# Kernel tuning notes

Measured on AMD Instinct MI355X. Metric: run time of the kernel, lower is better.

Reference implementation:

```python
import jax, jax.numpy as jnp
import numpy as np

# Model config (matches init_kwargs)
DIM = 2048
INTER = 1408          # moe_inter_dim
E = 16                # n_routed_experts
TOPK = 4              # n_activated_experts
G = 4                 # n_expert_groups
TOPK_G = 2            # n_limited_groups
N_SHARED = 2
SHARED_INTER = N_SHARED * INTER  # 2816
ROUTE_SCALE = 1.0


def setup_inputs() -> dict:
    key = jax.random.key(0)
    ks = jax.random.split(key, 8)
    s = 0.02
    x = jax.random.normal(ks[0], (1, 2048, DIM), dtype=jnp.float32)
    Wg = jax.random.normal(ks[1], (E, DIM), dtype=jnp.float32) * s      # gate weight
    W1 = jax.random.normal(ks[2], (E, INTER, DIM), dtype=jnp.float32) * s  # expert gate proj
    W3 = jax.random.normal(ks[3], (E, INTER, DIM), dtype=jnp.float32) * s  # expert up proj
    W2 = jax.random.normal(ks[4], (E, DIM, INTER), dtype=jnp.float32) * s  # expert down proj
    Ws1 = jax.random.normal(ks[5], (SHARED_INTER, DIM), dtype=jnp.float32) * s
    Ws3 = jax.random.normal(ks[6], (SHARED_INTER, DIM), dtype=jnp.float32) * s
    Ws2 = jax.random.normal(ks[7], (DIM, SHARED_INTER), dtype=jnp.float32) * s
    return {"x": x, "Wg": Wg, "W1": W1, "W3": W3, "W2": W2,
            "Ws1": Ws1, "Ws3": Ws3, "Ws2": Ws2}


def _moe_forward(x, Wg, W1, W3, W2, Ws1, Ws3, Ws2):
    B, S, D = x.shape
    xt = x.reshape(-1, D)              # [T, D]
    T = xt.shape[0]

    # ---- Gate: group-limited top-k routing (bias is None since dim != 7168) ----
    scores = jax.nn.softmax(xt @ Wg.T, axis=-1)          # [T, E]
    sg = scores.reshape(T, G, E // G)                    # [T, G, E/G]
    group_scores = sg.max(axis=-1)                       # amax per group
    gidx = jax.lax.top_k(group_scores, TOPK_G)[1]        # [T, TOPK_G]
    gmask = jax.nn.one_hot(gidx, G, dtype=jnp.float32).sum(axis=1) > 0  # [T, G] kept groups
    masked = jnp.where(gmask[:, :, None], sg, -jnp.inf).reshape(T, E)
    topi = jax.lax.top_k(masked, TOPK)[1]                # [T, TOPK] expert indices
    weights = jnp.take_along_axis(scores, topi, axis=1) * ROUTE_SCALE  # original_scores gather

    # ---- Routed experts: dense per-expert SwiGLU FFN, zero-weight combine ----
    # combine[t, e] = sum over k of weights[t, k] * (topi[t, k] == e)
    combine = jnp.zeros((T, E), xt.dtype).at[jnp.arange(T)[:, None], topi].add(weights)
    h = jax.nn.silu(jnp.einsum('td,eid->eti', xt, W1)) * jnp.einsum('td,eid->eti', xt, W3)
    expert_out = jnp.einsum('eti,edi->etd', h, W2)       # [E, T, D]
    y = jnp.einsum('etd,te->td', expert_out, combine)    # [T, D]

    # ---- Shared expert (applied to all tokens) ----
    z = (jax.nn.silu(xt @ Ws1.T) * (xt @ Ws3.T)) @ Ws2.T

    return (y + z).reshape(B, S, D)


def reference(x, Wg, W1, W3, W2, Ws1, Ws3, Ws2):
    return _moe_forward(x, Wg, W1, W3, W2, Ws1, Ws3, Ws2)
```

## Files before the change

kernel.cpp:

```cpp
#include <hip/hip_runtime.h>
#include <stdint.h>

#define D_MODEL  2048
#define N_INTER  1408
#define N_EXP    16
#define SH_INTER 2816
#define T_TOK    2048

typedef __attribute__((ext_vector_type(8))) short bf16x8;
typedef __attribute__((ext_vector_type(4))) float f32x4;

__device__ __forceinline__ unsigned short f2bf(float f){
  unsigned int b = __builtin_bit_cast(unsigned int, f);
  b = (b + 0x7FFFu + ((b >> 16) & 1u)) >> 16;
  return (unsigned short)b;
}

__global__ void cvt_bf16_kernel(const float* __restrict__ x,
                                unsigned short* __restrict__ o, int n4){
  const int i = blockIdx.x * blockDim.x + threadIdx.x;
  if (i >= n4) return;
  const float4 v = ((const float4*)x)[i];
  ushort4 u; u.x = f2bf(v.x); u.y = f2bf(v.y); u.z = f2bf(v.z); u.w = f2bf(v.w);
  ((ushort4*)o)[i] = u;
}

__global__ void gate_kernel(const float* __restrict__ x, const float* __restrict__ Wg,
                            int* __restrict__ cnt, int* __restrict__ list,
                            float* __restrict__ wlist){
  const int t = blockIdx.x;
  const int l = threadIdx.x;
  const int e = l & 15, q = l >> 4;
  const float* xr = x + (size_t)t * D_MODEL + q * 512;
  const float* wr = Wg + (size_t)e * D_MODEL + q * 512;
  float p = 0.f;
  #pragma unroll 4
  for (int i = 0; i < 512; i += 4){
    float4 xv = *(const float4*)(xr + i);
    float4 wv = *(const float4*)(wr + i);
    p += xv.x*wv.x + xv.y*wv.y + xv.z*wv.z + xv.w*wv.w;
  }
  p += __shfl_xor(p, 16);
  p += __shfl_xor(p, 32);
  float mx = p;
  for (int d = 1; d < 16; d <<= 1) mx = fmaxf(mx, __shfl_xor(mx, d));
  float ex = __expf(p - mx);
  float sum = ex;
  for (int d = 1; d < 16; d <<= 1) sum += __shfl_xor(sum, d);
  const float sc = ex / sum;
  float gm = fmaxf(sc, __shfl_xor(sc, 1));
  gm = fmaxf(gm, __shfl_xor(gm, 2));
  const float g0 = __shfl(gm, 0), g1 = __shfl(gm, 4),
              g2 = __shfl(gm, 8), g3 = __shfl(gm, 12);
  const int grp = e >> 2;
  const float gs[4] = {g0, g1, g2, g3};
  int grank = 0;
  #pragma unroll
  for (int j = 0; j < 4; ++j)
    if (gs[j] > gm || (gs[j] == gm && j < grp)) grank++;
  const float msc = (grank < 2) ? sc : -INFINITY;
  int erank = 0;
  #pragma unroll
  for (int j = 0; j < 16; ++j){
    const float oj = __shfl(msc, j);
    if (oj > msc || (oj == msc && j < e)) erank++;
  }
  if (q == 0 && erank < 4 && msc > -INFINITY){
    const int pos = atomicAdd(&cnt[e], 1);
    list[e * T_TOK + pos]  = (t << 2) | erank;
    wlist[e * T_TOK + pos] = sc;
  }
}

template<int MODE>
__global__ __launch_bounds__(256, 2)
void gemm_kernel(const unsigned short* __restrict__ A,
                 const float* __restrict__ B1,
                 const float* __restrict__ B3,
                 void* __restrict__ OutP,
                 const int* __restrict__ list,
                 const int* __restrict__ cnt,
                 const float* __restrict__ wlist,
                 int N, int K, int MT, int NT)
{
  constexpr bool GU     = (MODE == 0 || MODE == 1);
  constexpr bool GATHER = (MODE == 1 || MODE == 3);

  __shared__ unsigned short As [128 * 40];
  __shared__ unsigned short Bs1[128 * 40];
  __shared__ unsigned short Bs3[GU ? 128 * 40 : 8];

  const int nb  = gridDim.x;
  const int per = nb >> 3;
  const int gsw = (blockIdx.x & 7) * per + (blockIdx.x >> 3);
  const int mt   = gsw % MT;
  const int rest = gsw / MT;
  int nt, e;
  if (GATHER){ nt = rest % NT; e = rest / NT; } else { nt = rest; e = 0; }

  const int cntE = GATHER ? cnt[e] : (MT * 128);
  if (mt * 128 >= cntE) return;

  const size_t sB = (size_t)N * K;
  const float* b1 = B1 + (GATHER ? (size_t)e * sB : 0) + (size_t)(nt * 128) * K;
  const float* b3 = nullptr;
  if constexpr (GU) b3 = B3 + (GATHER ? (size_t)e * sB : 0) + (size_t)(nt * 128) * K;

  const int tid  = threadIdx.x;
  const int lrow = tid >> 2, seg0 = tid & 3;
  int arow0, arow1;
  if constexpr (GATHER){
    const int gr0 = mt * 128 + lrow, gr1 = gr0 + 64;
    const int p0 = min(gr0, cntE - 1), p1 = min(gr1, cntE - 1);
    const int e0 = list[e * T_TOK + p0], e1 = list[e * T_TOK + p1];
    arow0 = (MODE == 1) ? (e0 >> 2) : e0;
    arow1 = (MODE == 1) ? (e1 >> 2) : e1;
  } else { arow0 = mt * 128 + lrow; arow1 = arow0 + 64; }
  const unsigned short* pa0 = A + (size_t)arow0 * K + seg0 * 8;
  const unsigned short* pa1 = A + (size_t)arow1 * K + seg0 * 8;

  const int brow = tid >> 3, bseg = tid & 7;

  const int wid = tid >> 6, lane = tid & 63;
  const int wr = wid >> 1, wc = wid & 1;
  const int lr = lane & 15, lq = lane >> 4;

  f32x4 acc1[4][4];
  f32x4 acc3[GU ? 4 : 1][GU ? 4 : 1];
  const f32x4 zero = {0.f, 0.f, 0.f, 0.f};
  #pragma unroll
  for (int m = 0; m < 4; ++m)
    #pragma unroll
    for (int n = 0; n < 4; ++n){
      acc1[m][n] = zero;
      if constexpr (GU) acc3[m][n] = zero;
    }

  const int KT = K >> 5;
  for (int kt = 0; kt < KT; ++kt){
    const int k0 = kt << 5;
    __syncthreads();
    *(uint4*)(&As[lrow * 40 + seg0 * 8])        = *(const uint4*)(pa0 + k0);
    *(uint4*)(&As[(lrow + 64) * 40 + seg0 * 8]) = *(const uint4*)(pa1 + k0);
    #pragma unroll
    for (int j = 0; j < 4; ++j){
      const int row = brow + j * 32;
      const float4 v = *(const float4*)(b1 + (size_t)row * K + k0 + bseg * 4);
      ushort4 u; u.x = f2bf(v.x); u.y = f2bf(v.y); u.z = f2bf(v.z); u.w = f2bf(v.w);
      *(ushort4*)(&Bs1[row * 40 + bseg * 4]) = u;
      if constexpr (GU){
        const float4 w = *(const float4*)(b3 + (size_t)row * K + k0 + bseg * 4);
        ushort4 u3; u3.x = f2bf(w.x); u3.y = f2bf(w.y); u3.z = f2bf(w.z); u3.w = f2bf(w.w);
        *(ushort4*)(&Bs3[row * 40 + bseg * 4]) = u3;
      }
    }
    __syncthreads();

    bf16x8 af[4];
    #pragma unroll
    for (int m = 0; m < 4; ++m)
      af[m] = *(const bf16x8*)(&As[(wr * 64 + m * 16 + lr) * 40 + lq * 8]);
    #pragma unroll
    for (int n = 0; n < 4; ++n){
      const bf16x8 b1f = *(const bf16x8*)(&Bs1[(wc * 64 + n * 16 + lr) * 40 + lq * 8]);
      #pragma unroll
      for (int m = 0; m < 4; ++m)
        acc1[m][n] = __builtin_amdgcn_mfma_f32_16x16x32_bf16(af[m], b1f, acc1[m][n], 0, 0, 0);
      if constexpr (GU){
        const bf16x8 b3f = *(const bf16x8*)(&Bs3[(wc * 64 + n * 16 + lr) * 40 + lq * 8]);
        #pragma unroll
        for (int m = 0; m < 4; ++m)
          acc3[m][n] = __builtin_amdgcn_mfma_f32_16x16x32_bf16(af[m], b3f, acc3[m][n], 0, 0, 0);
      }
    }
  }

  float* Outf = (float*)OutP;
  unsigned short* Outh = (unsigned short*)OutP;
  #pragma unroll
  for (int m = 0; m < 4; ++m){
    #pragma unroll
    for (int r = 0; r < 4; ++r){
      const int grow = mt * 128 + wr * 64 + m * 16 + lq * 4 + r;
      int outrow; float wgt = 1.f; bool valid = true;
      if constexpr (GATHER){
        valid = grow < cntE;
        const int p = min(grow, cntE - 1);
        const int entry = list[e * T_TOK + p];
        if constexpr (MODE == 1) outrow = entry;
        else { outrow = entry >> 2; wgt = wlist[e * T_TOK + p]; }
      } else outrow = grow;
      if (!valid) continue;
      #pragma unroll
      for (int n = 0; n < 4; ++n){
        const int col = nt * 128 + wc * 64 + n * 16 + lr;
        if constexpr (GU){
          const float gv = acc1[m][n][r];
          const float uv = acc3[m][n][r];
          const float h = gv / (1.f + __expf(-gv)) * uv;
          Outh[(size_t)outrow * N + col] = f2bf(h);
        } else if constexpr (MODE == 2){
          Outf[(size_t)outrow * N + col] = acc1[m][n][r];
        } else {
          atomicAdd(&Outf[(size_t)outrow * N + col], acc1[m][n][r] * wgt);
        }
      }
    }
  }
}

extern "C" void kernel_launch(void* const* d_in, const int* in_sizes, int n_in,
                              void* d_out, int out_size, void* d_ws, size_t ws_size,
                              hipStream_t stream)
{
  const float* x   = (const float*)d_in[0];
  const float* Wg  = (const float*)d_in[1];
  const float* W1  = (const float*)d_in[2];
  const float* W3  = (const float*)d_in[3];
  const float* W2  = (const float*)d_in[4];
  const float* Ws1 = (const float*)d_in[5];
  const float* Ws3 = (const float*)d_in[6];
  const float* Ws2 = (const float*)d_in[7];
  float* out = (float*)d_out;

  char* ws = (char*)d_ws;
  int*            cnt   = (int*)ws;
  int*            list  = (int*)(ws + 4096);
  float*          wlist = (float*)(ws + 4096 + 16*T_TOK*4);
  unsigned short* xbf   = (unsigned short*)(ws + (size_t)(1  << 20));
  unsigned short* Hs    = (unsigned short*)(ws + (size_t)(9  << 20));
  unsigned short* H     = (unsigned short*)(ws + (size_t)(20 << 20));

  hipMemsetAsync(cnt, 0, 4096, stream);
  cvt_bf16_kernel<<<(T_TOK * D_MODEL / 4) / 256, 256, 0, stream>>>(x, xbf, T_TOK * D_MODEL / 4);
  gate_kernel<<<T_TOK, 64, 0, stream>>>(x, Wg, cnt, list, wlist);

  gemm_kernel<0><<<16 * 22, 256, 0, stream>>>(xbf, Ws1, Ws3, Hs,
                                              nullptr, nullptr, nullptr,
                                              SH_INTER, D_MODEL, 16, 22);
  gemm_kernel<2><<<16 * 16, 256, 0, stream>>>(Hs, Ws2, nullptr, out,
                                              nullptr, nullptr, nullptr,
                                              D_MODEL, SH_INTER, 16, 16);
  gemm_kernel<1><<<16 * 11 * 16, 256, 0, stream>>>(xbf, W1, W3, H,
                                                   list, cnt, nullptr,
                                                   N_INTER, D_MODEL, 16, 11);
  gemm_kernel<3><<<16 * 16 * 16, 256, 0, stream>>>(H, W2, nullptr, out,
                                                   list, cnt, wlist,
                                                   D_MODEL, N_INTER, 16, 16);
}
```

Measured before the change: 754.4 us.

## Split gate/up GEMMs, double-buffer A via global_load_lds, replace atomics with combine kernel

Replaces the fused gate+up GEMM with a single-B GEMM kernel that uses a 128x64 tile. The A operand is double-buffered through direct global-to-LDS loads, B is register-prefetched, and both use an XOR-swizzled LDS layout. SwiGLU moves into a separate elementwise kernel. The routed down-projection now writes per-slot bf16 outputs, which a combine kernel sums with the routing weights instead of using atomicAdd. This removes atomics and bank conflicts and overlaps loads with MFMA, at the cost of extra intermediate bf16 traffic, extra launches, and an extra bf16 rounding of the expert outputs.

```diff
diff --git a/kernel.cpp b/kernel.cpp
--- a/kernel.cpp
+++ b/kernel.cpp
@@ -3,9 +3,9 @@
 
 #define D_MODEL  2048
 #define N_INTER  1408
-#define N_EXP    16
 #define SH_INTER 2816
 #define T_TOK    2048
+#define NSLOT    (T_TOK * 4)
 
 typedef __attribute__((ext_vector_type(8))) short bf16x8;
 typedef __attribute__((ext_vector_type(4))) float f32x4;
@@ -15,6 +15,14 @@
   b = (b + 0x7FFFu + ((b >> 16) & 1u)) >> 16;
   return (unsigned short)b;
 }
+__device__ __forceinline__ float bf2f(unsigned short h){
+  unsigned int b = ((unsigned int)h) << 16;
+  return __builtin_bit_cast(float, b);
+}
+
+#define GLOAD16(gp, lp) __builtin_amdgcn_global_load_lds( \
+    (const __attribute__((address_space(1))) unsigned int*)(gp), \
+    (__attribute__((address_space(3))) unsigned int*)(lp), 16, 0, 0)
 
 __global__ void cvt_bf16_kernel(const float* __restrict__ x,
                                 unsigned short* __restrict__ o, int n4){
@@ -27,7 +35,7 @@
 
 __global__ void gate_kernel(const float* __restrict__ x, const float* __restrict__ Wg,
                             int* __restrict__ cnt, int* __restrict__ list,
-                            float* __restrict__ wlist){
+                            float* __restrict__ wslot){
   const int t = blockIdx.x;
   const int l = threadIdx.x;
   const int e = l & 15, q = l >> 4;
@@ -67,146 +75,187 @@
   }
   if (q == 0 && erank < 4 && msc > -INFINITY){
     const int pos = atomicAdd(&cnt[e], 1);
-    list[e * T_TOK + pos]  = (t << 2) | erank;
-    wlist[e * T_TOK + pos] = sc;
+    const int slot = (t << 2) | erank;
+    list[e * T_TOK + pos] = slot;
+    wslot[slot] = sc;
   }
 }
 
 template<int MODE>
 __global__ __launch_bounds__(256, 2)
-void gemm_kernel(const unsigned short* __restrict__ A,
-                 const float* __restrict__ B1,
-                 const float* __restrict__ B3,
-                 void* __restrict__ OutP,
-                 const int* __restrict__ list,
-                 const int* __restrict__ cnt,
-                 const float* __restrict__ wlist,
-                 int N, int K, int MT, int NT)
+void gemm2_kernel(const unsigned short* __restrict__ A,
+                  const float* __restrict__ B,
+                  void* __restrict__ OutP,
+                  const int* __restrict__ list,
+                  const int* __restrict__ cnt,
+                  int N, int K, int MT, int NT)
 {
-  constexpr bool GU     = (MODE == 0 || MODE == 1);
-  constexpr bool GATHER = (MODE == 1 || MODE == 3);
-
-  __shared__ unsigned short As [128 * 40];
-  __shared__ unsigned short Bs1[128 * 40];
-  __shared__ unsigned short Bs3[GU ? 128 * 40 : 8];
-
-  const int nb  = gridDim.x;
-  const int per = nb >> 3;
+  constexpr bool GATHER = (MODE >= 2);
+  __shared__ unsigned short As[2 * 128 * 32];
+  __shared__ unsigned short Bs[64 * 32];
+
+  const int per = gridDim.x >> 3;
   const int gsw = (blockIdx.x & 7) * per + (blockIdx.x >> 3);
   const int mt   = gsw % MT;
   const int rest = gsw / MT;
-  int nt, e;
-  if (GATHER){ nt = rest % NT; e = rest / NT; } else { nt = rest; e = 0; }
+  const int nt = GATHER ? (rest % NT) : rest;
+  const int e  = GATHER ? (rest / NT) : 0;
 
   const int cntE = GATHER ? cnt[e] : (MT * 128);
   if (mt * 128 >= cntE) return;
 
-  const size_t sB = (size_t)N * K;
-  const float* b1 = B1 + (GATHER ? (size_t)e * sB : 0) + (size_t)(nt * 128) * K;
-  const float* b3 = nullptr;
-  if constexpr (GU) b3 = B3 + (GATHER ? (size_t)e * sB : 0) + (size_t)(nt * 128) * K;
-
-  const int tid  = threadIdx.x;
-  const int lrow = tid >> 2, seg0 = tid & 3;
-  int arow0, arow1;
+  const int tid = threadIdx.x, wid = tid >> 6, lane = tid & 63;
+
+  const int rt0 = 32 * wid + (lane >> 2), rt1 = rt0 + 16;
+  int ar0, ar1;
   if constexpr (GATHER){
-    const int gr0 = mt * 128 + lrow, gr1 = gr0 + 64;
-    const int p0 = min(gr0, cntE - 1), p1 = min(gr1, cntE - 1);
+    const int lim = cntE - 1;
+    int p0 = mt * 128 + rt0; p0 = p0 < lim ? p0 : lim;
+    int p1 = mt * 128 + rt1; p1 = p1 < lim ? p1 : lim;
     const int e0 = list[e * T_TOK + p0], e1 = list[e * T_TOK + p1];
-    arow0 = (MODE == 1) ? (e0 >> 2) : e0;
-    arow1 = (MODE == 1) ? (e1 >> 2) : e1;
-  } else { arow0 = mt * 128 + lrow; arow1 = arow0 + 64; }
-  const unsigned short* pa0 = A + (size_t)arow0 * K + seg0 * 8;
-  const unsigned short* pa1 = A + (size_t)arow1 * K + seg0 * 8;
-
-  const int brow = tid >> 3, bseg = tid & 7;
-
-  const int wid = tid >> 6, lane = tid & 63;
-  const int wr = wid >> 1, wc = wid & 1;
-  const int lr = lane & 15, lq = lane >> 4;
-
-  f32x4 acc1[4][4];
-  f32x4 acc3[GU ? 4 : 1][GU ? 4 : 1];
+    ar0 = (MODE == 2) ? (e0 >> 2) : e0;
+    ar1 = (MODE == 2) ? (e1 >> 2) : e1;
+  } else { ar0 = mt * 128 + rt0; ar1 = mt * 128 + rt1; }
+  const unsigned short* pa0 = A + (size_t)ar0 * K + (((lane & 3) ^ ((rt0 >> 1) & 3)) << 3);
+  const unsigned short* pa1 = A + (size_t)ar1 * K + (((lane & 3) ^ ((rt1 >> 1) & 3)) << 3);
+  unsigned short* const asBase = &As[0];
+  const int aW0 = (32 * wid) * 32, aW1 = (32 * wid + 16) * 32;
+  const int bufStride = 128 * 32;
+
+  const int brow = tid >> 2, bsl = tid & 3;
+  const float* pb = B + (GATHER ? (size_t)e * N * K : 0)
+                  + (size_t)(nt * 64 + brow) * K
+                  + (((bsl ^ ((brow >> 1) & 3))) << 3);
+  unsigned short* const bsDst = &Bs[brow * 32 + (bsl << 3)];
+
+  const int wr = wid >> 1, wc = wid & 1, lr = lane & 15, lq = lane >> 4;
+  const int fx = ((lq ^ ((lr >> 1) & 3)) << 3);
+  int aoff[4], boff[2];
+  #pragma unroll
+  for (int m = 0; m < 4; ++m) aoff[m] = (wr * 64 + m * 16 + lr) * 32 + fx;
+  #pragma unroll
+  for (int n = 0; n < 2; ++n) boff[n] = (wc * 32 + n * 16 + lr) * 32 + fx;
+
+  f32x4 acc[4][2];
   const f32x4 zero = {0.f, 0.f, 0.f, 0.f};
   #pragma unroll
   for (int m = 0; m < 4; ++m)
     #pragma unroll
-    for (int n = 0; n < 4; ++n){
-      acc1[m][n] = zero;
-      if constexpr (GU) acc3[m][n] = zero;
+    for (int n = 0; n < 2; ++n) acc[m][n] = zero;
+
+  const int KT = K >> 5;
+  GLOAD16(pa0, asBase + aW0);
+  GLOAD16(pa1, asBase + aW1);
+  float4 bp0 = *(const float4*)pb;
+  float4 bp1 = *(const float4*)(pb + 4);
+  pa0 += 32; pa1 += 32; pb += 32;
+  int cur = 0;
+
+  for (int kt = 0; kt < KT; ++kt){
+    __syncthreads();
+    bf16x8 ub;
+    ub[0] = (short)f2bf(bp0.x); ub[1] = (short)f2bf(bp0.y);
+    ub[2] = (short)f2bf(bp0.z); ub[3] = (short)f2bf(bp0.w);
+    ub[4] = (short)f2bf(bp1.x); ub[5] = (short)f2bf(bp1.y);
+    ub[6] = (short)f2bf(bp1.z); ub[7] = (short)f2bf(bp1.w);
+    *(bf16x8*)bsDst = ub;
+    __syncthreads();
+    if (kt + 1 < KT){
+      const int nxt = cur ^ 1;
+      GLOAD16(pa0, asBase + nxt * bufStride + aW0);
+      GLOAD16(pa1, asBase + nxt * bufStride + aW1);
+      bp0 = *(const float4*)pb;
+      bp1 = *(const float4*)(pb + 4);
+      pa0 += 32; pa1 += 32; pb += 32;
     }
-
-  const int KT = K >> 5;
-  for (int kt = 0; kt < KT; ++kt){
-    const int k0 = kt << 5;
-    __syncthreads();
-    *(uint4*)(&As[lrow * 40 + seg0 * 8])        = *(const uint4*)(pa0 + k0);
-    *(uint4*)(&As[(lrow + 64) * 40 + seg0 * 8]) = *(const uint4*)(pa1 + k0);
+    const unsigned short* aCur = asBase + cur * bufStride;
+    bf16x8 af0 = *(const bf16x8*)(aCur + aoff[0]);
+    bf16x8 af1 = *(const bf16x8*)(aCur + aoff[1]);
+    bf16x8 af2 = *(const bf16x8*)(aCur + aoff[2]);
+    bf16x8 af3 = *(const bf16x8*)(aCur + aoff[3]);
+    bf16x8 bf0 = *(const bf16x8*)(&Bs[0] + boff[0]);
+    bf16x8 bf1 = *(const bf16x8*)(&Bs[0] + boff[1]);
+    acc[0][0] = __builtin_amdgcn_mfma_f32_16x16x32_bf16(af0, bf0, acc[0][0], 0, 0, 0);
+    acc[1][0] = __builtin_amdgcn_mfma_f32_16x16x32_bf16(af1, bf0, acc[1][0], 0, 0, 0);
+    acc[2][0] = __builtin_amdgcn_mfma_f32_16x16x32_bf16(af2, bf0, acc[2][0], 0, 0, 0);
+    acc[3][0] = __builtin_amdgcn_mfma_f32_16x16x32_bf16(af3, bf0, acc[3][0], 0, 0, 0);
+    acc[0][1] = __builtin_amdgcn_mfma_f32_16x16x32_bf16(af0, bf1, acc[0][1], 0, 0, 0);
+    acc[1][1] = __builtin_amdgcn_mfma_f32_16x16x32_bf16(af1, bf1, acc[1][1], 0, 0, 0);
+    acc[2][1] = __builtin_amdgcn_mfma_f32_16x16x32_bf16(af2, bf1, acc[2][1], 0, 0, 0);
+    acc[3][1] = __builtin_amdgcn_mfma_f32_16x16x32_bf16(af3, bf1, acc[3][1], 0, 0, 0);
+    cur ^= 1;
+  }
+
+  const int colBase = nt * 64 + wc * 32;
+  if constexpr (MODE == 1){
+    float* O = (float*)OutP;
     #pragma unroll
-    for (int j = 0; j < 4; ++j){
-      const int row = brow + j * 32;
-      const float4 v = *(const float4*)(b1 + (size_t)row * K + k0 + bseg * 4);
-      ushort4 u; u.x = f2bf(v.x); u.y = f2bf(v.y); u.z = f2bf(v.z); u.w = f2bf(v.w);
-      *(ushort4*)(&Bs1[row * 40 + bseg * 4]) = u;
-      if constexpr (GU){
-        const float4 w = *(const float4*)(b3 + (size_t)row * K + k0 + bseg * 4);
-        ushort4 u3; u3.x = f2bf(w.x); u3.y = f2bf(w.y); u3.z = f2bf(w.z); u3.w = f2bf(w.w);
-        *(ushort4*)(&Bs3[row * 40 + bseg * 4]) = u3;
+    for (int m = 0; m < 4; ++m){
+      #pragma unroll
+      for (int r = 0; r < 4; ++r){
+        const int grow = mt * 128 + wr * 64 + m * 16 + lq * 4 + r;
+        float* op = O + (size_t)grow * N + colBase;
+        op[lr]      = acc[m][0][r];
+        op[16 + lr] = acc[m][1][r];
       }
     }
-    __syncthreads();
-
-    bf16x8 af[4];
+  } else {
+    unsigned short* O = (unsigned short*)OutP;
     #pragma unroll
-    for (int m = 0; m < 4; ++m)
-      af[m] = *(const bf16x8*)(&As[(wr * 64 + m * 16 + lr) * 40 + lq * 8]);
-    #pragma unroll
-    for (int n = 0; n < 4; ++n){
-      const bf16x8 b1f = *(const bf16x8*)(&Bs1[(wc * 64 + n * 16 + lr) * 40 + lq * 8]);
+    for (int m = 0; m < 4; ++m){
       #pragma unroll
-      for (int m = 0; m < 4; ++m)
-        acc1[m][n] = __builtin_amdgcn_mfma_f32_16x16x32_bf16(af[m], b1f, acc1[m][n], 0, 0, 0);
-      if constexpr (GU){
-        const bf16x8 b3f = *(const bf16x8*)(&Bs3[(wc * 64 + n * 16 + lr) * 40 + lq * 8]);
-        #pragma unroll
-        for (int m = 0; m < 4; ++m)
-          acc3[m][n] = __builtin_amdgcn_mfma_f32_16x16x32_bf16(af[m], b3f, acc3[m][n], 0, 0, 0);
+      for (int r = 0; r < 4; ++r){
+        const int grow = mt * 128 + wr * 64 + m * 16 + lq * 4 + r;
+        int orow;
+        if constexpr (GATHER){
+          if (grow >= cntE) continue;
+          orow = list[e * T_TOK + grow];
+        } else orow = grow;
+        unsigned short* op = O + (size_t)orow * N + colBase;
+        op[lr]      = f2bf(acc[m][0][r]);
+        op[16 + lr] = f2bf(acc[m][1][r]);
       }
     }
   }
-
-  float* Outf = (float*)OutP;
-  unsigned short* Outh = (unsigned short*)OutP;
-  #pragma unroll
-  for (int m = 0; m < 4; ++m){
+}
+
+__global__ void swiglu_kernel(const unsigned short* __restrict__ G,
+                              const unsigned short* __restrict__ U,
+                              unsigned short* __restrict__ H, int n8){
+  const int i = blockIdx.x * blockDim.x + threadIdx.x;
+  if (i >= n8) return;
+  const bf16x8 g = ((const bf16x8*)G)[i];
+  const bf16x8 u = ((const bf16x8*)U)[i];
+  bf16x8 h;
+  #pragma unroll
+  for (int j = 0; j < 8; ++j){
+    const float gv = bf2f((unsigned short)g[j]);
+    const float uv = bf2f((unsigned short)u[j]);
+    h[j] = (short)f2bf(gv / (1.f + __expf(-gv)) * uv);
+  }
+  ((bf16x8*)H)[i] = h;
+}
+
+__global__ void combine_kernel(const unsigned short* __restrict__ H2,
+                               const float* __restrict__ wslot,
+                               float* __restrict__ out){
+  const int t = blockIdx.x;
+  const int c = threadIdx.x * 8;
+  float w[4];
+  #pragma unroll
+  for (int k = 0; k < 4; ++k) w[k] = wslot[t * 4 + k];
+  float* o = out + (size_t)t * D_MODEL + c;
+  float a[8];
+  #pragma unroll
+  for (int j = 0; j < 8; ++j) a[j] = o[j];
+  #pragma unroll
+  for (int k = 0; k < 4; ++k){
+    const bf16x8 hv = *(const bf16x8*)(H2 + (size_t)(t * 4 + k) * D_MODEL + c);
     #pragma unroll
-    for (int r = 0; r < 4; ++r){
-      const int grow = mt * 128 + wr * 64 + m * 16 + lq * 4 + r;
-      int outrow; float wgt = 1.f; bool valid = true;
-      if constexpr (GATHER){
-        valid = grow < cntE;
-        const int p = min(grow, cntE - 1);
-        const int entry = list[e * T_TOK + p];
-        if constexpr (MODE == 1) outrow = entry;
-        else { outrow = entry >> 2; wgt = wlist[e * T_TOK + p]; }
-      } else outrow = grow;
-      if (!valid) continue;
-      #pragma unroll
-      for (int n = 0; n < 4; ++n){
-        const int col = nt * 128 + wc * 64 + n * 16 + lr;
-        if constexpr (GU){
-          const float gv = acc1[m][n][r];
-          const float uv = acc3[m][n][r];
-          const float h = gv / (1.f + __expf(-gv)) * uv;
-          Outh[(size_t)outrow * N + col] = f2bf(h);
-        } else if constexpr (MODE == 2){
-          Outf[(size_t)outrow * N + col] = acc1[m][n][r];
-        } else {
-          atomicAdd(&Outf[(size_t)outrow * N + col], acc1[m][n][r] * wgt);
-        }
-      }
-    }
-  }
+    for (int j = 0; j < 8; ++j) a[j] += w[k] * bf2f((unsigned short)hv[j]);
+  }
+  #pragma unroll
+  for (int j = 0; j < 8; ++j) o[j] = a[j];
 }
 
 extern "C" void kernel_launch(void* const* d_in, const int* in_sizes, int n_in,
@@ -224,27 +273,38 @@
   float* out = (float*)d_out;
 
   char* ws = (char*)d_ws;
-  int*            cnt   = (int*)ws;
+  int*            cnt   = (int*)(ws);
   int*            list  = (int*)(ws + 4096);
-  float*          wlist = (float*)(ws + 4096 + 16*T_TOK*4);
-  unsigned short* xbf   = (unsigned short*)(ws + (size_t)(1  << 20));
-  unsigned short* Hs    = (unsigned short*)(ws + (size_t)(9  << 20));
-  unsigned short* H     = (unsigned short*)(ws + (size_t)(20 << 20));
+  float*          wslot = (float*)(ws + 4096 + 131072);
+  unsigned short* xbf = (unsigned short*)(ws + ((size_t)1  << 20));
+  unsigned short* Gs  = (unsigned short*)(ws + ((size_t)10 << 20));
+  unsigned short* Us  = (unsigned short*)(ws + ((size_t)22 << 20));
+  unsigned short* Hs  = (unsigned short*)(ws + ((size_t)34 << 20));
+  unsigned short* Gr  = (unsigned short*)(ws + ((size_t)46 << 20));
+  unsigned short* Ur  = (unsigned short*)(ws + ((size_t)70 << 20));
+  unsigned short* Hr  = (unsigned short*)(ws + ((size_t)94 << 20));
+  unsigned short* H2  = (unsigned short*)(ws + ((size_t)118 << 20));
 
   hipMemsetAsync(cnt, 0, 4096, stream);
   cvt_bf16_kernel<<<(T_TOK * D_MODEL / 4) / 256, 256, 0, stream>>>(x, xbf, T_TOK * D_MODEL / 4);
-  gate_kernel<<<T_TOK, 64, 0, stream>>>(x, Wg, cnt, list, wlist);
-
-  gemm_kernel<0><<<16 * 22, 256, 0, stream>>>(xbf, Ws1, Ws3, Hs,
-                                              nullptr, nullptr, nullptr,
-                                              SH_INTER, D_MODEL, 16, 22);
-  gemm_kernel<2><<<16 * 16, 256, 0, stream>>>(Hs, Ws2, nullptr, out,
-                                              nullptr, nullptr, nullptr,
-                                              D_MODEL, SH_INTER, 16, 16);
-  gemm_kernel<1><<<16 * 11 * 16, 256, 0, stream>>>(xbf, W1, W3, H,
-                                                   list, cnt, nullptr,
-                                                   N_INTER, D_MODEL, 16, 11);
-  gemm_kernel<3><<<16 * 16 * 16, 256, 0, stream>>>(H, W2, nullptr, out,
-                                                   list, cnt, wlist,
-                                                   D_MODEL, N_INTER, 16, 16);
-}
+  gate_kernel<<<T_TOK, 64, 0, stream>>>(x, Wg, cnt, list, wslot);
+
+  gemm2_kernel<0><<<16 * 44, 256, 0, stream>>>(xbf, Ws1, Gs, nullptr, nullptr,
+                                               SH_INTER, D_MODEL, 16, 44);
+  gemm2_kernel<0><<<16 * 44, 256, 0, stream>>>(xbf, Ws3, Us, nullptr, nullptr,
+                                               SH_INTER, D_MODEL, 16, 44);
+  swiglu_kernel<<<(T_TOK * SH_INTER / 8) / 256, 256, 0, stream>>>(Gs, Us, Hs,
+                                               T_TOK * SH_INTER / 8);
+  gemm2_kernel<1><<<16 * 32, 256, 0, stream>>>(Hs, Ws2, out, nullptr, nullptr,
+                                               D_MODEL, SH_INTER, 16, 32);
+
+  gemm2_kernel<2><<<16 * 22 * 16, 256, 0, stream>>>(xbf, W1, Gr, list, cnt,
+                                                    N_INTER, D_MODEL, 16, 22);
+  gemm2_kernel<2><<<16 * 22 * 16, 256, 0, stream>>>(xbf, W3, Ur, list, cnt,
+                                                    N_INTER, D_MODEL, 16, 22);
+  swiglu_kernel<<<(NSLOT * N_INTER / 8) / 256, 256, 0, stream>>>(Gr, Ur, Hr,
+                                                    NSLOT * N_INTER / 8);
+  gemm2_kernel<3><<<16 * 32 * 16, 256, 0, stream>>>(Hr, W2, H2, list, cnt,
+                                                    D_MODEL, N_INTER, 16, 32);
+  combine_kernel<<<T_TOK, 256, 0, stream>>>(H2, wslot, out);
+}
```

After: 894.7 us. +18.6%, slower.
